# Performance work log

Measured on AMD Instinct MI355X. Metric: run time of the kernel, lower is better.

## Reference

```python
import jax, jax.numpy as jnp
import numpy as np

B, T, C = 8, 2048, 1024
HS = 128           # head_size
N_TERMS = 2
THETA = 10000.0


def _rope_tables(dim, end):
    freqs = 1.0 / (THETA ** (jnp.arange(0, dim, 2, dtype=jnp.float32) / dim))  # [dim/2]
    ang = jnp.arange(end, dtype=jnp.float32)[:, None] * freqs[None, :]          # [end, dim/2]
    return jnp.cos(ang), jnp.sin(ang)


def _apply_rope(x, cos, sin):
    # x: [..., T, D]; pairs are interleaved (x0,x1),(x2,x3),...
    xr = x[..., 0::2]
    xi = x[..., 1::2]
    or_ = xr * cos - xi * sin
    oi = xr * sin + xi * cos
    return jnp.stack([or_, oi], axis=-1).reshape(x.shape)


def setup_inputs() -> dict:
    key = jax.random.key(0)
    ks = jax.random.split(key, 6)
    x = jax.random.normal(ks[0], (B, T, C), dtype=jnp.float32)
    Wq = jax.random.normal(ks[1], (N_TERMS, C, HS), dtype=jnp.float32) * 0.02
    Wk = jax.random.normal(ks[2], (N_TERMS, C, HS), dtype=jnp.float32) * 0.02
    Wv = jax.random.normal(ks[3], (C, 2 * HS), dtype=jnp.float32) * 0.02
    lambda_q = jax.random.normal(ks[4], (N_TERMS, HS), dtype=jnp.float32) * 0.1
    lambda_k = jax.random.normal(ks[5], (N_TERMS, HS), dtype=jnp.float32) * 0.1
    return {"x": x, "Wq": Wq, "Wk": Wk, "Wv": Wv,
            "lambda_q": lambda_q, "lambda_k": lambda_k, "layer_idx": 3}


def reference(x, Wq, Wk, Wv, lambda_q, lambda_k, layer_idx):
    Bx, Tx, Cx = x.shape
    n = Wq.shape[0]
    scale = 1.0 / (HS ** 0.5)

    v = x @ Wv                                   # [B,T,2*HS]
    q = jnp.einsum('btc,ncd->nbtd', x, Wq)       # [n,B,T,HS]
    k = jnp.einsum('btc,ncd->nbtd', x, Wk)

    cos, sin = _rope_tables(HS, Tx)              # [T, HS/2]
    q = _apply_rope(q, cos, sin)
    k = _apply_rope(k, cos, sin)

    att = jnp.einsum('nbtd,nbsd->nbts', q, k) * scale  # [n,B,T,T]
    causal = jnp.tril(jnp.ones((Tx, Tx), dtype=bool))
    att = jnp.where(causal, att, -jnp.inf)
    att = jax.nn.softmax(att, axis=-1)

    # lambda values
    lam_init = 0.8 - 0.6 * jnp.exp(-0.3 * (jnp.float32(layer_idx) - 1.0))
    e = jnp.mean(jnp.exp(lambda_q * lambda_k), axis=-1)         # [n]
    e_prev = jnp.concatenate([jnp.zeros((1,), e.dtype), e[:-1]])
    lam = e - e_prev + lam_init                                 # [n]
    signs = jnp.where(jnp.arange(n) % 2 == 1, -1.0, 1.0)

    diff_att = jnp.einsum('n,nbts->bts', signs * lam, att)      # [B,T,T]
    out = diff_att @ v                                          # [B,T,2*HS]
    return out
```

## Files before the change

kernel.cpp:

```cpp
#include <hip/hip_runtime.h>
#include <math.h>

#define B_DIM 8
#define T_DIM 2048
#define C_DIM 1024
#define HS_DIM 128
#define VD 256
#define M_DIM (B_DIM * T_DIM)
#define QK_ELEMS (M_DIM * HS_DIM)
#define SCALE 0.088388347648318447f
#define LOG_THETA 9.210340371976184f

#define QB_OFF   0u
#define KB_OFF   4194304u
#define VT_OFF   8388608u
#define WT_OFF   12582912u
#define XBH_OFF  13369344u
#define LAM_OFF  21757952u
#define XSPLIT_ELEMS 8388608u

typedef short s8v   __attribute__((ext_vector_type(8)));
typedef float f32x4 __attribute__((ext_vector_type(4)));
typedef float f32x16 __attribute__((ext_vector_type(16)));

__device__ __forceinline__ unsigned int bf16_rne(float f) {
    unsigned int u = __float_as_uint(f);
    return (u + 0x7fffu + ((u >> 16) & 1u)) >> 16;
}
__device__ __forceinline__ unsigned int pack_bf2(float lo, float hi) {
    return bf16_rne(lo) | (bf16_rne(hi) << 16);
}
__device__ __forceinline__ void async_cp16(const unsigned short* g, unsigned short* l) {
    __builtin_amdgcn_global_load_lds(
        (const __attribute__((address_space(1))) unsigned int*)g,
        (__attribute__((address_space(3))) unsigned int*)l, 16, 0, 0);
}

__global__ void lam_kernel(const float* __restrict__ lq, const float* __restrict__ lk,
                           const int* __restrict__ lidx, float* __restrict__ lam_out) {
    int t = threadIdx.x;
    float s0 = expf(lq[t] * lk[t]) + expf(lq[t + 64] * lk[t + 64]);
    float s1 = expf(lq[128 + t] * lk[128 + t]) + expf(lq[192 + t] * lk[192 + t]);
    #pragma unroll
    for (int off = 32; off > 0; off >>= 1) {
        s0 += __shfl_down(s0, off);
        s1 += __shfl_down(s1, off);
    }
    if (t == 0) {
        float e0 = s0 * (1.0f / 128.0f);
        float e1 = s1 * (1.0f / 128.0f);
        float li = 0.8f - 0.6f * expf(-0.3f * ((float)lidx[0] - 1.0f));
        lam_out[0] = e0 + li;
        lam_out[1] = -(e1 - e0 + li);
    }
}

__global__ __launch_bounds__(256) void cast_x_kernel(const float* __restrict__ x,
                                                     unsigned short* __restrict__ lo,
                                                     unsigned short* __restrict__ hi) {
    const size_t i8 = ((size_t)blockIdx.x * 256 + threadIdx.x) * 8;
    float4 a = *(const float4*)(x + i8);
    float4 b = *(const float4*)(x + i8 + 4);
    uint4 u;
    u.x = pack_bf2(a.x, a.y); u.y = pack_bf2(a.z, a.w);
    u.z = pack_bf2(b.x, b.y); u.w = pack_bf2(b.z, b.w);
    unsigned short* dst = (i8 < XSPLIT_ELEMS) ? (lo + i8) : (hi + (i8 - XSPLIT_ELEMS));
    *(uint4*)dst = u;
}

__global__ __launch_bounds__(256) void cast_wt_kernel(
    const float* __restrict__ Wq, const float* __restrict__ Wk,
    const float* __restrict__ Wv, unsigned short* __restrict__ wt) {
    __shared__ float tile[32][33];
    const int t = threadIdx.x;
    const int n0 = blockIdx.x * 32;
    const int k0 = blockIdx.y * 32;
    const int seg = n0 >> 7;
    const int nl = t & 31;
    const int ng = n0 + nl;
    const float* src; int ld;
    if (seg < 2)      { src = Wq + (size_t)seg * (C_DIM * HS_DIM) + (ng & 127); ld = 128; }
    else if (seg < 4) { src = Wk + (size_t)(seg - 2) * (C_DIM * HS_DIM) + (ng & 127); ld = 128; }
    else              { src = Wv + (ng - 512); ld = 256; }
    #pragma unroll
    for (int rep = 0; rep < 4; ++rep) {
        int kl = (t >> 5) + rep * 8;
        tile[kl][nl] = src[(size_t)(k0 + kl) * ld];
    }
    __syncthreads();
    unsigned int* wt32 = (unsigned int*)wt;
    #pragma unroll
    for (int rep = 0; rep < 2; ++rep) {
        int nl2 = (t >> 4) + rep * 16;
        int k2 = (t & 15) * 2;
        unsigned int u = pack_bf2(tile[k2][nl2], tile[k2 + 1][nl2]);
        wt32[((size_t)(n0 + nl2) * 1024 + k0 + k2) >> 1] = u;
    }
}

__global__ __launch_bounds__(256) void gemm_kernel(
    const unsigned short* __restrict__ xlo, const unsigned short* __restrict__ xhi,
    const unsigned short* __restrict__ wt,
    unsigned short* __restrict__ qo, unsigned short* __restrict__ ko,
    unsigned short* __restrict__ vo) {
    __shared__ unsigned short As[128 * 32];
    __shared__ unsigned short Bs[128 * 32];

    const int t = threadIdx.x;
    const int wv = t >> 6, lane = t & 63;
    const int quad = lane >> 4, l15 = lane & 15;
    const int m0 = blockIdx.x * 128;
    const int n0 = blockIdx.y * 128;
    const int wr = wv >> 1, wc = wv & 1;

    const unsigned short* xbase = (m0 < 8192)
        ? (xlo + (size_t)m0 * C_DIM) : (xhi + (size_t)(m0 - 8192) * C_DIM);

    f32x4 acc[4][4];
    #pragma unroll
    for (int i = 0; i < 4; ++i)
        #pragma unroll
        for (int j = 0; j < 4; ++j) acc[i][j] = (f32x4){0.f, 0.f, 0.f, 0.f};

    const int srow = lane >> 2;
    const int skof = (lane & 3) * 8;

    for (int k0 = 0; k0 < C_DIM; k0 += 32) {
        #pragma unroll
        for (int j = 0; j < 2; ++j) {
            const int c = wv * 2 + j;
            async_cp16(xbase + (size_t)(c * 16 + srow) * C_DIM + k0 + skof, As + c * 512);
        }
        #pragma unroll
        for (int j = 0; j < 2; ++j) {
            const int c = wv * 2 + j;
            async_cp16(wt + (size_t)(n0 + c * 16 + srow) * C_DIM + k0 + skof, Bs + c * 512);
        }
        __syncthreads();
        s8v af[4], bf[4];
        #pragma unroll
        for (int i = 0; i < 4; ++i)
            af[i] = *(const s8v*)&As[(wr * 64 + i * 16 + l15) * 32 + quad * 8];
        #pragma unroll
        for (int j = 0; j < 4; ++j)
            bf[j] = *(const s8v*)&Bs[(wc * 64 + j * 16 + l15) * 32 + quad * 8];
        #pragma unroll
        for (int i = 0; i < 4; ++i)
            #pragma unroll
            for (int j = 0; j < 4; ++j)
                acc[i][j] = __builtin_amdgcn_mfma_f32_16x16x32_bf16(af[i], bf[j], acc[i][j], 0, 0, 0);
        __syncthreads();
    }

    const int seg = n0 >> 7;
    if (seg < 4) {
        unsigned short* dstbuf = ((seg < 2) ? qo : ko) + (size_t)(seg & 1) * QK_ELEMS;
        float freqj[4];
        #pragma unroll
        for (int j = 0; j < 4; ++j) {
            const int d = wc * 64 + j * 16 + l15;
            freqj[j] = __expf((float)(d >> 1) * (-LOG_THETA / 64.f));
        }
        const int odd = lane & 1;
        #pragma unroll
        for (int i = 0; i < 4; ++i) {
            #pragma unroll
            for (int e = 0; e < 4; ++e) {
                const int m = m0 + wr * 64 + i * 16 + quad * 4 + e;
                const float trow = (float)(m & (T_DIM - 1));
                unsigned int* p32 = (unsigned int*)(dstbuf + (size_t)m * HS_DIM);
                #pragma unroll
                for (int j = 0; j < 4; ++j) {
                    const int d = wc * 64 + j * 16 + l15;
                    const float val = acc[i][j][e];
                    const float other = __shfl_xor(val, 1);
                    float sn_, cs_;
                    __sincosf(trow * freqj[j], &sn_, &cs_);
                    const float out = val * cs_ + (odd ? other * sn_ : -other * sn_);
                    const float out2 = __shfl_xor(out, 1);
                    if (!odd) p32[d >> 1] = pack_bf2(out, out2);
                }
            }
        }
    } else {
        const int bq = m0 >> 11;
        const int tbase = m0 & (T_DIM - 1);
        unsigned int* vT32 = (unsigned int*)vo;
        #pragma unroll
        for (int j = 0; j < 4; ++j) {
            const int d = (seg - 4) * 128 + wc * 64 + j * 16 + l15;
            const size_t rowbase = (size_t)(bq * VD + d) * (T_DIM / 2);
            #pragma unroll
            for (int i = 0; i < 4; ++i) {
                const int tok = tbase + wr * 64 + i * 16 + quad * 4;
                uint2 u;
                u.x = pack_bf2(acc[i][j][0], acc[i][j][1]);
                u.y = pack_bf2(acc[i][j][2], acc[i][j][3]);
                *(uint2*)&vT32[rowbase + (tok >> 1)] = u;
            }
        }
    }
}

#define OSTR 260
#define PSTR 72
#define K_OFF 0
#define V_OFF 32768
#define P_OFF 65536
#define SM_TOTAL 74752

__global__ __launch_bounds__(256, 2) void attn_kernel(
    const unsigned short* __restrict__ qg, const unsigned short* __restrict__ kg,
    const unsigned short* __restrict__ vg, const float* __restrict__ lam,
    float* __restrict__ outp) {
    __shared__ __align__(16) unsigned char smem[SM_TOTAL];
    unsigned short* Ks = (unsigned short*)(smem + K_OFF);
    unsigned short* Vt = (unsigned short*)(smem + V_OFF);
    unsigned short* Ps = (unsigned short*)(smem + P_OFF);
    float* Ol = (float*)smem;
    float* Lsum = (float*)(smem + P_OFF);

    const int t = threadIdx.x;
    const int id = blockIdx.x;
    const int b = id & 7;
    const int sidx = id >> 3;
    const int strip = (sidx < 32) ? (63 - sidx) : (sidx - 32);
    const int q0 = strip * 32;
    const int nt = (strip >> 1) + 1;

    const int w = t >> 6, lane = t & 63;
    const int l31 = lane & 31, lh = lane >> 5;
    const int term = w & 1;
    const int kh = w >> 1;

    const float cn = lam[term];

    const unsigned short* qrow = qg
        + ((size_t)(term * B_DIM + b) * T_DIM + q0 + l31) * HS_DIM + lh * 8;
    s8v qa[8];
    #pragma unroll
    for (int ks = 0; ks < 8; ++ks)
        qa[ks] = *(const s8v*)(qrow + ks * 16);

    f32x16 o[4];
    #pragma unroll
    for (int dt = 0; dt < 4; ++dt)
        #pragma unroll
        for (int r = 0; r < 16; ++r) o[dt][r] = 0.f;
    float l_acc[16];
    #pragma unroll
    for (int r = 0; r < 16; ++r) l_acc[r] = 0.f;

    for (int it = 0; it < nt; ++it) {
        const int s0 = it * 64;
        #pragma unroll
        for (int oo = 0; oo < 8; ++oo) {
            const int idx = (w * 8 + oo) * 64 + lane;
            const int rfull = idx >> 4;
            const int cc = idx & 15;
            const int ccs = cc ^ (rfull & 7);
            const int n = rfull >> 6, r = rfull & 63;
            async_cp16(kg + ((size_t)(n * B_DIM + b) * T_DIM + s0 + r) * HS_DIM + ccs * 8,
                       Ks + (w * 8 + oo) * 512);
        }
        #pragma unroll
        for (int oo = 0; oo < 8; ++oo) {
            const int idx = (w * 8 + oo) * 64 + lane;
            const int d = idx >> 3;
            const int cc = idx & 7;
            const int ccs = cc ^ (d & 7);
            async_cp16(vg + ((size_t)(b * VD + d) * T_DIM + s0) + ccs * 8,
                       Vt + (w * 8 + oo) * 512);
        }
        __syncthreads();

        f32x16 sc;
        #pragma unroll
        for (int r = 0; r < 16; ++r) sc[r] = 0.f;
        {
            const int krow = term * 64 + kh * 32 + l31;
            const unsigned short* kb = Ks + krow * 128;
            const int sw = krow & 7;
            #pragma unroll
            for (int ks = 0; ks < 8; ++ks) {
                s8v kf = *(const s8v*)(kb + (((ks * 2 + lh) ^ sw) << 3));
                sc = __builtin_amdgcn_mfma_f32_32x32x16_bf16(qa[ks], kf, sc, 0, 0, 0);
            }
        }
        const int key = s0 + kh * 32 + l31;
        #pragma unroll
        for (int r = 0; r < 16; ++r) {
            const int row = (r & 3) + 8 * (r >> 2) + 4 * lh;
            const float p = (key <= q0 + row) ? __expf(sc[r] * SCALE) : 0.f;
            l_acc[r] += p;
            Ps[(term * 32 + row) * PSTR + kh * 32 + l31] = (unsigned short)bf16_rne(p);
        }
        __syncthreads();

        #pragma unroll
        for (int ks = 0; ks < 4; ++ks) {
            s8v pa = *(const s8v*)&Ps[(term * 32 + l31) * PSTR + ks * 16 + lh * 8];
            #pragma unroll
            for (int dt = 0; dt < 4; ++dt) {
                const int d = kh * 128 + dt * 32 + l31;
                s8v vb = *(const s8v*)(Vt + d * 64 + (((ks * 2 + lh) ^ (d & 7)) << 3));
                o[dt] = __builtin_amdgcn_mfma_f32_32x32x16_bf16(pa, vb, o[dt], 0, 0, 0);
            }
        }
        __syncthreads();
    }

    #pragma unroll
    for (int r = 0; r < 16; ++r) {
        float lt = l_acc[r];
        #pragma unroll
        for (int off = 1; off < 32; off <<= 1) lt += __shfl_xor(lt, off);
        if (l31 == 0) {
            const int row = (r & 3) + 8 * (r >> 2) + 4 * lh;
            Lsum[(term * 2 + kh) * 32 + row] = lt;
        }
    }
    __syncthreads();
    float inv[16];
    #pragma unroll
    for (int r = 0; r < 16; ++r) {
        const int row = (r & 3) + 8 * (r >> 2) + 4 * lh;
        inv[r] = cn / (Lsum[(term * 2 + 0) * 32 + row] + Lsum[(term * 2 + 1) * 32 + row]);
    }

    if (term) {
        #pragma unroll
        for (int dt = 0; dt < 4; ++dt)
            #pragma unroll
            for (int r = 0; r < 16; ++r) {
                const int row = (r & 3) + 8 * (r >> 2) + 4 * lh;
                Ol[row * OSTR + kh * 128 + dt * 32 + l31] = o[dt][r] * inv[r];
            }
    }
    __syncthreads();
    if (!term) {
        #pragma unroll
        for (int dt = 0; dt < 4; ++dt)
            #pragma unroll
            for (int r = 0; r < 16; ++r) {
                const int row = (r & 3) + 8 * (r >> 2) + 4 * lh;
                Ol[row * OSTR + kh * 128 + dt * 32 + l31] += o[dt][r] * inv[r];
            }
    }
    __syncthreads();
    #pragma unroll
    for (int rep = 0; rep < 8; ++rep) {
        int idx = t + rep * 256;
        int row = idx >> 6, c4 = idx & 63;
        float4 val = *(const float4*)&Ol[row * OSTR + c4 * 4];
        *(float4*)&outp[((size_t)(b * T_DIM + q0 + row)) * VD + c4 * 4] = val;
    }
}

extern "C" void kernel_launch(void* const* d_in, const int* in_sizes, int n_in,
                              void* d_out, int out_size, void* d_ws, size_t ws_size,
                              hipStream_t stream) {
    const float* x  = (const float*)d_in[0];
    const float* Wq = (const float*)d_in[1];
    const float* Wk = (const float*)d_in[2];
    const float* Wv = (const float*)d_in[3];
    const float* lq = (const float*)d_in[4];
    const float* lk = (const float*)d_in[5];
    const int* lidx = (const int*)d_in[6];

    unsigned short* ws = (unsigned short*)d_ws;
    unsigned short* qb   = ws + QB_OFF;
    unsigned short* kb   = ws + KB_OFF;
    unsigned short* vTb  = ws + VT_OFF;
    unsigned short* wtb  = ws + WT_OFF;
    unsigned short* xbhi = ws + XBH_OFF;
    float* lamb = (float*)(ws + LAM_OFF);
    unsigned short* xblo = (unsigned short*)d_out;
    (void)ws_size; (void)in_sizes; (void)n_in; (void)out_size;

    lam_kernel<<<dim3(1), dim3(64), 0, stream>>>(lq, lk, lidx, lamb);
    cast_x_kernel<<<dim3(8192), dim3(256), 0, stream>>>(x, xblo, xbhi);
    cast_wt_kernel<<<dim3(24, 32), dim3(256), 0, stream>>>(Wq, Wk, Wv, wtb);
    gemm_kernel<<<dim3(128, 6), dim3(256), 0, stream>>>(xblo, xbhi, wtb, qb, kb, vTb);
    attn_kernel<<<dim3(512), dim3(256), 0, stream>>>(qb, kb, vTb, lamb, (float*)d_out);
}
```

Before: 234.2 us.

## Split PV output columns across waves so each wave holds both terms

The P·V stage now gives each wave a 64-column slice of the output for both terms, instead of one term over 128 columns. Each wave can then combine the two terms in registers, which removes the shared-memory reduction epilogue and its two extra barriers. The cost is loading both P fragments per k-step and writing to global as scattered scalar stores instead of coalesced float4 stores.

```diff
diff --git a/kernel.cpp b/kernel.cpp
--- a/kernel.cpp
+++ b/kernel.cpp
@@ -202,7 +202,6 @@
     }
 }
 
-#define OSTR 260
 #define PSTR 72
 #define K_OFF 0
 #define V_OFF 32768
@@ -217,7 +216,6 @@
     unsigned short* Ks = (unsigned short*)(smem + K_OFF);
     unsigned short* Vt = (unsigned short*)(smem + V_OFF);
     unsigned short* Ps = (unsigned short*)(smem + P_OFF);
-    float* Ol = (float*)smem;
     float* Lsum = (float*)(smem + P_OFF);
 
     const int t = threadIdx.x;
@@ -233,7 +231,7 @@
     const int term = w & 1;
     const int kh = w >> 1;
 
-    const float cn = lam[term];
+    const float c0 = lam[0], c1 = lam[1];
 
     const unsigned short* qrow = qg
         + ((size_t)(term * B_DIM + b) * T_DIM + q0 + l31) * HS_DIM + lh * 8;
@@ -242,11 +240,13 @@
     for (int ks = 0; ks < 8; ++ks)
         qa[ks] = *(const s8v*)(qrow + ks * 16);
 
-    f32x16 o[4];
-    #pragma unroll
-    for (int dt = 0; dt < 4; ++dt)
-        #pragma unroll
-        for (int r = 0; r < 16; ++r) o[dt][r] = 0.f;
+    f32x16 o[2][2];
+    #pragma unroll
+    for (int tm = 0; tm < 2; ++tm)
+        #pragma unroll
+        for (int dt = 0; dt < 2; ++dt)
+            #pragma unroll
+            for (int r = 0; r < 16; ++r) o[tm][dt][r] = 0.f;
     float l_acc[16];
     #pragma unroll
     for (int r = 0; r < 16; ++r) l_acc[r] = 0.f;
@@ -299,12 +299,14 @@
 
         #pragma unroll
         for (int ks = 0; ks < 4; ++ks) {
-            s8v pa = *(const s8v*)&Ps[(term * 32 + l31) * PSTR + ks * 16 + lh * 8];
-            #pragma unroll
-            for (int dt = 0; dt < 4; ++dt) {
-                const int d = kh * 128 + dt * 32 + l31;
-                s8v vb = *(const s8v*)(Vt + d * 64 + (((ks * 2 + lh) ^ (d & 7)) << 3));
-                o[dt] = __builtin_amdgcn_mfma_f32_32x32x16_bf16(pa, vb, o[dt], 0, 0, 0);
+            const s8v pa0 = *(const s8v*)&Ps[(0 * 32 + l31) * PSTR + ks * 16 + lh * 8];
+            const s8v pa1 = *(const s8v*)&Ps[(1 * 32 + l31) * PSTR + ks * 16 + lh * 8];
+            #pragma unroll
+            for (int dt = 0; dt < 2; ++dt) {
+                const int d = w * 64 + dt * 32 + l31;
+                const s8v vb = *(const s8v*)(Vt + d * 64 + (((ks * 2 + lh) ^ (d & 7)) << 3));
+                o[0][dt] = __builtin_amdgcn_mfma_f32_32x32x16_bf16(pa0, vb, o[0][dt], 0, 0, 0);
+                o[1][dt] = __builtin_amdgcn_mfma_f32_32x32x16_bf16(pa1, vb, o[1][dt], 0, 0, 0);
             }
         }
         __syncthreads();
@@ -321,39 +323,23 @@
         }
     }
     __syncthreads();
-    float inv[16];
+    float inv0[16], inv1[16];
     #pragma unroll
     for (int r = 0; r < 16; ++r) {
         const int row = (r & 3) + 8 * (r >> 2) + 4 * lh;
-        inv[r] = cn / (Lsum[(term * 2 + 0) * 32 + row] + Lsum[(term * 2 + 1) * 32 + row]);
-    }
-
-    if (term) {
-        #pragma unroll
-        for (int dt = 0; dt < 4; ++dt)
-            #pragma unroll
-            for (int r = 0; r < 16; ++r) {
-                const int row = (r & 3) + 8 * (r >> 2) + 4 * lh;
-                Ol[row * OSTR + kh * 128 + dt * 32 + l31] = o[dt][r] * inv[r];
-            }
-    }
-    __syncthreads();
-    if (!term) {
-        #pragma unroll
-        for (int dt = 0; dt < 4; ++dt)
-            #pragma unroll
-            for (int r = 0; r < 16; ++r) {
-                const int row = (r & 3) + 8 * (r >> 2) + 4 * lh;
-                Ol[row * OSTR + kh * 128 + dt * 32 + l31] += o[dt][r] * inv[r];
-            }
-    }
-    __syncthreads();
-    #pragma unroll
-    for (int rep = 0; rep < 8; ++rep) {
-        int idx = t + rep * 256;
-        int row = idx >> 6, c4 = idx & 63;
-        float4 val = *(const float4*)&Ol[row * OSTR + c4 * 4];
-        *(float4*)&outp[((size_t)(b * T_DIM + q0 + row)) * VD + c4 * 4] = val;
+        inv0[r] = c0 / (Lsum[0 * 32 + row] + Lsum[1 * 32 + row]);
+        inv1[r] = c1 / (Lsum[2 * 32 + row] + Lsum[3 * 32 + row]);
+    }
+
+    #pragma unroll
+    for (int dt = 0; dt < 2; ++dt) {
+        const int d = w * 64 + dt * 32 + l31;
+        #pragma unroll
+        for (int r = 0; r < 16; ++r) {
+            const int row = (r & 3) + 8 * (r >> 2) + 4 * lh;
+            const float val = o[0][dt][r] * inv0[r] + o[1][dt][r] * inv1[r];
+            outp[((size_t)(b * T_DIM + q0 + row)) * VD + d] = val;
+        }
     }
 }
 
```

Result: no change. 235.3 us (+0.5%).
